# Performance work log

Hardware: AMD Instinct MI355X
Metric: run time of the kernel (lower is better)

## Reference

```python
import jax, jax.numpy as jnp
import numpy as np

B, N, D = 16, 1024, 512
NH = 8
HD = D // NH
K_DEFAULT, K_MAX = 4, 6
PROX_THRESH = 20.0
LN_EPS = 1e-5


def _linear_params(key, din, dout):
    kw, kb = jax.random.split(key)
    lim = 1.0 / np.sqrt(din)
    W = jax.random.uniform(kw, (din, dout), jnp.float32, -lim, lim)
    b = jax.random.uniform(kb, (dout,), jnp.float32, -lim, lim)
    return W, b


def setup_inputs() -> dict:
    key = jax.random.key(0)
    ks = jax.random.split(key, 16)
    agent_repr_1 = jax.random.normal(ks[0], (B, N, D), jnp.float32)
    ego_distance = jax.random.uniform(ks[1], (B, N), jnp.float32) * 100.0  # meters
    ego_mask = jax.random.uniform(ks[2], (B, N), jnp.float32)  # soft ego indicator (torch casts bool->float)
    ego_speed = jax.random.uniform(ks[3], (B,), jnp.float32) * 10.0
    Wq, bq = _linear_params(ks[4], D, D)
    Wk, bk = _linear_params(ks[5], D, D)
    Wv, bv = _linear_params(ks[6], D, D)
    Weq, beq = _linear_params(ks[7], D, D)
    Wek, bek = _linear_params(ks[8], D, D)  # defined in module but unused in forward
    Wev, bev = _linear_params(ks[9], D, D)  # defined in module but unused in forward
    Wd1, bd1 = _linear_params(ks[10], 2, D // 4)
    Wd2, bd2 = _linear_params(ks[11], D // 4, NH)
    ln_g = jnp.ones((D,), jnp.float32)
    ln_b = jnp.zeros((D,), jnp.float32)
    return dict(agent_repr_1=agent_repr_1, ego_distance=ego_distance, ego_mask=ego_mask,
                ego_speed=ego_speed, Wq=Wq, bq=bq, Wk=Wk, bk=bk, Wv=Wv, bv=bv,
                Weq=Weq, beq=beq, Wek=Wek, bek=bek, Wev=Wev, bev=bev,
                Wd1=Wd1, bd1=bd1, Wd2=Wd2, bd2=bd2, ln_g=ln_g, ln_b=ln_b)


def _compute_K(ego_speed, ego_distance):
    # deterministic lookup table; concrete python int (mirrors .item() in torch)
    d = np.asarray(ego_distance)
    s = np.asarray(ego_speed)
    density = (d < PROX_THRESH).astype(np.float32).sum(-1) / max(d.shape[-1], 1)
    K = K_DEFAULT
    if float(s.mean()) > 15.0:
        K = min(K + 1, K_MAX)
    if float(density.mean()) > 0.5:
        K = min(K + 1, K_MAX)
    return K


def _layernorm(x, g, b):
    mu = jnp.mean(x, -1, keepdims=True)
    var = jnp.var(x, -1, keepdims=True)
    return (x - mu) * jax.lax.rsqrt(var + LN_EPS) * g + b


def reference(agent_repr_1, ego_distance, ego_mask, ego_speed,
              Wq, bq, Wk, bk, Wv, bv, Weq, beq, Wek, bek, Wev, bev,
              Wd1, bd1, Wd2, bd2, ln_g, ln_b):
    K = min(_compute_K(ego_speed, ego_distance), N - 1)
    if K <= 0:
        return _layernorm(agent_repr_1, ln_g, ln_b)
    # top-K nearest neighbors by ego distance, excluding self
    dist = jnp.broadcast_to(ego_distance[:, None, :], (B, N, N))  # row i: candidate distances
    dist = jnp.where(jnp.eye(N, dtype=bool)[None], jnp.inf, dist)
    _, topk_idx = jax.lax.top_k(-dist, K)  # [B,N,K] smallest distances
    gathered = jax.vmap(lambda xb, ib: xb[ib])(agent_repr_1, topk_idx)  # [B,N,K,D]
    is_ego = ego_mask[..., None]
    Q = (1.0 - is_ego) * (agent_repr_1 @ Wq + bq) + is_ego * (agent_repr_1 @ Weq + beq)
    Km = gathered @ Wk + bk
    Vm = gathered @ Wv + bv
    Qh = Q.reshape(B, N, NH, HD).transpose(0, 2, 1, 3)          # [B,H,N,hd]
    Kh = Km.reshape(B, N, K, NH, HD).transpose(0, 3, 1, 2, 4)   # [B,H,N,K,hd]
    Vh = Vm.reshape(B, N, K, NH, HD).transpose(0, 3, 1, 2, 4)
    scores = jnp.einsum('bhnd,bhnkd->bhnk', Qh, Kh) / np.sqrt(HD)
    q_dist = jnp.broadcast_to(ego_distance[:, :, None], (B, N, K))
    k_dist = jnp.take_along_axis(jnp.broadcast_to(ego_distance[:, None, :], (B, N, N)), topk_idx, axis=2)
    dist_pair = jnp.stack([q_dist, k_dist], -1)                 # [B,N,K,2]
    bias = jax.nn.relu(dist_pair @ Wd1 + bd1) @ Wd2 + bd2       # [B,N,K,H]
    scores = scores * bias.transpose(0, 3, 1, 2)                # multiplicative distance bias
    attn = jax.nn.softmax(scores, axis=-1)
    attn_out = jnp.einsum('bhnk,bhnkd->bhnd', attn, Vh)
    attn_out = attn_out.transpose(0, 2, 1, 3).reshape(B, N, D)
    return _layernorm(agent_repr_1 + attn_out, ln_g, ln_b)
```

## Files before the change

kernel.cpp:

```cpp
#include <hip/hip_runtime.h>
#include <math.h>

constexpr int CB  = 16;
constexpr int CN  = 1024;
constexpr int CD  = 512;
constexpr int KM1 = 7;
constexpr int RB  = 32;

typedef __attribute__((ext_vector_type(8))) short bf8;
typedef __attribute__((ext_vector_type(4))) float f32x4;
typedef __attribute__((ext_vector_type(4))) unsigned short us4;

__device__ inline float bf2f(unsigned short u) {
    union { unsigned int i; float f; } v; v.i = ((unsigned)u) << 16; return v.f;
}
__device__ inline unsigned short f2bf(float f) {
    union { unsigned int i; float f; } v; v.f = f;
    unsigned r = v.i + 0x7FFFu + ((v.i >> 16) & 1u);
    return (unsigned short)(r >> 16);
}
__device__ inline unsigned int cvtpk(float lo, float hi) {
    unsigned int r;
    asm("v_cvt_pk_bf16_f32 %0, %1, %2" : "=v"(r) : "v"(lo), "v"(hi));
    return r;
}
__device__ inline bf8 pack8(float4 x, float4 y) {
    union { bf8 v; unsigned int u[4]; } r;
    r.u[0] = cvtpk(x.x, x.y); r.u[1] = cvtpk(x.z, x.w);
    r.u[2] = cvtpk(y.x, y.y); r.u[3] = cvtpk(y.z, y.w);
    return r.v;
}
__device__ inline us4 pack4(float4 x) {
    union { us4 v; unsigned int u[2]; } r;
    r.u[0] = cvtpk(x.x, x.y); r.u[1] = cvtpk(x.z, x.w);
    return r.v;
}

__global__ __launch_bounds__(256) void k_pre(
    const float* __restrict__ dist, const float* __restrict__ speed,
    const float* __restrict__ Wk, const float* __restrict__ Wv,
    int* __restrict__ Kout,
    int* __restrict__ candIdx, float* __restrict__ candDist,
    unsigned short* __restrict__ WkT, unsigned short* __restrict__ WvT) {
    int t = threadIdx.x;
    int bid = blockIdx.x;

    if (bid < 16) {
        __shared__ float sdist[CN];
        __shared__ unsigned long long red64[4];
        int b = bid;
        for (int i = t; i < CN; i += 256) sdist[i] = dist[b * CN + i];
        __syncthreads();
        for (int sel = 0; sel < KM1; sel++) {
            unsigned long long best = 0xFFFFFFFFFFFFFFFFull;
            for (int i = t; i < CN; i += 256) {
                unsigned long long key =
                    ((unsigned long long)__float_as_uint(sdist[i]) << 32) | (unsigned)i;
                best = best < key ? best : key;
            }
#pragma unroll
            for (int off = 32; off; off >>= 1) {
                unsigned long long o = __shfl_xor(best, off);
                best = best < o ? best : o;
            }
            if ((t & 63) == 0) red64[t >> 6] = best;
            __syncthreads();
            if (t == 0) {
                unsigned long long m0 = red64[0] < red64[1] ? red64[0] : red64[1];
                unsigned long long m1 = red64[2] < red64[3] ? red64[2] : red64[3];
                unsigned long long m = m0 < m1 ? m0 : m1;
                int idx = (int)(unsigned)(m & 0xFFFFFFFFu);
                candIdx[b * KM1 + sel]  = idx;
                candDist[b * KM1 + sel] = __uint_as_float((unsigned)(m >> 32));
                sdist[idx] = 3.4e38f;
            }
            __syncthreads();
        }
        return;
    }
    if (bid < 144) {
        __shared__ unsigned short tile[64][68];
        int b2 = bid - 16;
        int kt = b2 & 7, ct = (b2 >> 3) & 7, mat = b2 >> 6;
        const float* W = mat ? Wv : Wk;
        unsigned short* WT = mat ? WvT : WkT;
        int k0 = kt * 64, c0 = ct * 64;
#pragma unroll
        for (int p = 0; p < 4; p++) {
            int kr = p * 16 + (t >> 4);
            int cc = (t & 15) * 4;
            float4 v = *(const float4*)(W + (size_t)(k0 + kr) * CD + c0 + cc);
            *(us4*)&tile[kr][cc] = pack4(v);
        }
        __syncthreads();
#pragma unroll
        for (int p = 0; p < 4; p++) {
            int cr = p * 16 + (t >> 4);
            int kk = (t & 15) * 4;
            us4 o;
            o.x = tile[kk + 0][cr];
            o.y = tile[kk + 1][cr];
            o.z = tile[kk + 2][cr];
            o.w = tile[kk + 3][cr];
            *(us4*)(WT + (size_t)(c0 + cr) * CD + k0 + kk) = o;
        }
        return;
    }
    {
        __shared__ int red[256];
        int cnt = 0;
        for (int i = t; i < CB * CN; i += 256) cnt += (dist[i] < 20.0f) ? 1 : 0;
        red[t] = cnt;
        __syncthreads();
        for (int s = 128; s > 0; s >>= 1) {
            if (t < s) red[t] += red[t + s];
            __syncthreads();
        }
        if (t == 0) {
            float ss = 0.f;
            for (int i = 0; i < CB; i++) ss += speed[i];
            int K = 4;
            if (ss / (float)CB > 15.0f) K = (K + 1 > 6) ? 6 : K + 1;
            float density = (float)red[0] / (float)(CB * CN);
            if (density > 0.5f) K = (K + 1 > 6) ? 6 : K + 1;
            if (K > CN - 1) K = CN - 1;
            if (K < 0) K = 0;
            *Kout = K;
        }
    }
}

__global__ __launch_bounds__(256) void k_mid(
    const float* __restrict__ X,
    const unsigned short* __restrict__ WkT, const float* __restrict__ bk,
    const unsigned short* __restrict__ WvT, const float* __restrict__ bv,
    const float* __restrict__ Wq, const float* __restrict__ bq,
    const float* __restrict__ Weq, const float* __restrict__ beq,
    const int* __restrict__ candIdx,
    unsigned short* __restrict__ VcB, float* __restrict__ S0,
    unsigned short* __restrict__ Y,
    unsigned short* __restrict__ X2) {
    int t = threadIdx.x;
    int bid = blockIdx.x;
    __shared__ unsigned short sbuf[RB][520];

    if (bid >= 384) {
        int tileId = bid - 384;
        int b = tileId >> 5, rblk = tileId & 31;
        int row0 = b * CN + rblk * RB;
        for (int idx = t; idx < RB * 128; idx += 256) {
            int r = idx >> 7, c4 = idx & 127;
            float4 xv = *(const float4*)(X + (size_t)(row0 + r) * CD + c4 * 4);
            *(us4*)&sbuf[r][c4 * 4] = pack4(xv);
        }
        __syncthreads();
        unsigned short* dst = X2 + (size_t)tileId * 16384;
#pragma unroll
        for (int it = 0; it < 8; it++) {
            int unit = t + it * 256;
            int r = unit & 31, kg = (unit >> 5) & 3, s = unit >> 7;
            const unsigned short* src = &sbuf[r][s * 32 + kg * 8];
            us4 lo = *(const us4*)src;
            us4 hi = *(const us4*)(src + 4);
            *(us4*)(dst + (size_t)unit * 8)     = lo;
            *(us4*)(dst + (size_t)unit * 8 + 4) = hi;
        }
        return;
    }

    int b = (bid < 128) ? (bid >> 3) : ((bid - 128) >> 4);
    for (int i = t; i < 16 * 128; i += 256) {
        int m = i >> 7, c4 = i & 127;
        float4 xv = {0.f, 0.f, 0.f, 0.f};
        if (m < KM1)
            xv = *(const float4*)(X + (size_t)(b * CN + candIdx[b * KM1 + m]) * CD + c4 * 4);
        *(us4*)&sbuf[m][c4 * 4] = pack4(xv);
    }
    __syncthreads();

    int w = t >> 6, lane = t & 63, lr = lane & 15, kg = lane >> 4;

    if (bid < 128) {
        int ny = bid & 7;
        int c = ny * 64 + w * 16 + lr;
        const unsigned short* wtp = WvT + (size_t)c * CD + kg * 8;
        f32x4 acc = {0.f, 0.f, 0.f, 0.f};
#pragma unroll
        for (int s = 0; s < 16; s++) {
            bf8 bfr = *(const bf8*)(wtp + s * 32);
            bf8 a   = *(const bf8*)&sbuf[lr][s * 32 + kg * 8];
            acc = __builtin_amdgcn_mfma_f32_16x16x32_bf16(a, bfr, acc, 0, 0, 0);
        }
        float bv_ = bv[c];
#pragma unroll
        for (int q = 0; q < 4; q++) {
            int m = kg * 4 + q;
            if (m < KM1)
                VcB[(size_t)(b * KM1 + m) * CD + c] = f2bf(acc[q] + bv_);
        }
        return;
    }

    int rem = (bid - 128) & 15;
    int h = rem >> 1, half = rem & 1;
    __shared__ unsigned short sKc16[16][68];
    __shared__ float sKcf[KM1][64];

    {
        int c = h * 64 + w * 16 + lr;
        const unsigned short* wtp = WkT + (size_t)c * CD + kg * 8;
        f32x4 acc = {0.f, 0.f, 0.f, 0.f};
#pragma unroll
        for (int s = 0; s < 16; s++) {
            bf8 bfr = *(const bf8*)(wtp + s * 32);
            bf8 a   = *(const bf8*)&sbuf[lr][s * 32 + kg * 8];
            acc = __builtin_amdgcn_mfma_f32_16x16x32_bf16(a, bfr, acc, 0, 0, 0);
        }
        float bk_ = bk[c];
        int cl = w * 16 + lr;
#pragma unroll
        for (int q = 0; q < 4; q++) {
            int m = kg * 4 + q;
            float val = (m < KM1) ? (acc[q] + bk_) : 0.f;
            sKc16[m][cl] = f2bf(val);
            if (m < KM1) sKcf[m][cl] = val;
        }
    }
    __syncthreads();

    if (half == 0 && t < 14) {
        int mat = t / 7, m = t % 7;
        const float* bias = mat ? beq : bq;
        float s = 0.f;
        for (int c = 0; c < 64; c++) s = fmaf(bias[h * 64 + c], sKcf[m][c], s);
        S0[((b * 2 + mat) * KM1 + m) * 8 + h] = s;
    }

    bf8 a0 = *(const bf8*)&sKc16[lr][kg * 8];
    bf8 a1 = *(const bf8*)&sKc16[lr][32 + kg * 8];
    unsigned short* Y2b = Y + (size_t)b * 64 * 112 * 8;
#pragma unroll
    for (int mat = 0; mat < 2; mat++) {
        const float* W = mat ? Weq : Wq;
#pragma unroll
        for (int nt = 0; nt < 4; nt++) {
            int n0 = (half * 16 + w * 4 + nt) * 16;
            const float* wp = W + (size_t)(n0 + lr) * CD + h * 64 + kg * 8;
            float4 f0 = *(const float4*)(wp);
            float4 f1 = *(const float4*)(wp + 4);
            float4 f2 = *(const float4*)(wp + 32);
            float4 f3 = *(const float4*)(wp + 36);
            f32x4 acc = {0.f, 0.f, 0.f, 0.f};
            acc = __builtin_amdgcn_mfma_f32_16x16x32_bf16(a0, pack8(f0, f1), acc, 0, 0, 0);
            acc = __builtin_amdgcn_mfma_f32_16x16x32_bf16(a1, pack8(f2, f3), acc, 0, 0, 0);
            int k_out = n0 + lr;
            int k8 = k_out >> 3, krem = k_out & 7;
#pragma unroll
            for (int q = 0; q < 4; q++) {
                int m = kg * 4 + q;
                if (m < KM1) {
                    int n = mat * 56 + m * 8 + h;
                    Y2b[((size_t)k8 * 112 + n) * 8 + krem] = f2bf(acc[q]);
                }
            }
        }
    }
}

__global__ __launch_bounds__(512) void k_attn(
    const float* __restrict__ X, const float* __restrict__ dist,
    const float* __restrict__ mask,
    const float* __restrict__ Wd1, const float* __restrict__ bd1,
    const float* __restrict__ Wd2, const float* __restrict__ bd2,
    const float* __restrict__ lng, const float* __restrict__ lnb,
    const int* __restrict__ Kp, const int* __restrict__ candIdx,
    const float* __restrict__ candDist,
    const unsigned short* __restrict__ VcB, const float* __restrict__ S0,
    const unsigned short* __restrict__ Y,
    const unsigned short* __restrict__ X2, int useX2,
    float* __restrict__ out) {

    __shared__ float sS[RB][116];
    __shared__ unsigned short sVc[KM1][520];
    __shared__ float sW7[RB][8][8];
    __shared__ float sBias[RB][6][2][8];
    __shared__ int   snbr[RB][6];
    __shared__ float skd[RB][6];
    __shared__ float srd[RB];
    __shared__ float sE[RB];
    __shared__ float sS0[112];

    int t = threadIdx.x;
    int hw = blockIdx.x;
    int bid = (hw & 7) * 64 + (hw >> 3);
    int b = bid >> 5, rblk = bid & 31;
    int row0 = b * CN + rblk * RB;
    int K = *Kp;

    for (int idx = t; idx < KM1 * 128; idx += 512) {
        int m = idx >> 7, c4 = idx & 127;
        *(us4*)&sVc[m][c4 * 4] =
            *(const us4*)(VcB + (size_t)(b * KM1 + m) * CD + c4 * 4);
    }
    if (t < 112) sS0[t] = S0[b * 112 + t];
    if (t < RB) {
        int i = rblk * RB + t;
        sE[t]  = mask[b * CN + i];
        srd[t] = dist[b * CN + i];
        int cnt = 0;
        for (int m = 0; m <= K && cnt < K; m++) {
            int c = candIdx[b * KM1 + m];
            if (c != i) { snbr[t][cnt] = m; skd[t][cnt] = candDist[b * KM1 + m]; cnt++; }
        }
    }
    __syncthreads();

    int w = t >> 6;
    if (w < 4) {
        int lane = t & 63, lr = lane & 15, kg = lane >> 4;
        f32x4 acc00 = {0.f, 0.f, 0.f, 0.f}, acc10 = acc00, acc01 = acc00, acc11 = acc00;
        bool has2 = (w < 3);
        const unsigned short* ypk = Y + ((size_t)b * 64 * 112 + (size_t)kg * 112 + (w * 16 + lr)) * 8;
        __builtin_amdgcn_s_setprio(1);
        if (useX2) {
            const unsigned short* x2s = X2 + (size_t)bid * 16384 + kg * 256 + lr * 8;
#pragma unroll
            for (int s = 0; s < 16; s++) {
                const unsigned short* xp = x2s + s * 1024;
                bf8 a0 = *(const bf8*)xp;
                bf8 a1 = *(const bf8*)(xp + 128);
                const unsigned short* ys = ypk + (size_t)s * 4 * 112 * 8;
                bf8 b0 = *(const bf8*)ys;
                acc00 = __builtin_amdgcn_mfma_f32_16x16x32_bf16(a0, b0, acc00, 0, 0, 0);
                acc10 = __builtin_amdgcn_mfma_f32_16x16x32_bf16(a1, b0, acc10, 0, 0, 0);
                if (has2) {
                    bf8 b1 = *(const bf8*)(ys + 512);
                    acc01 = __builtin_amdgcn_mfma_f32_16x16x32_bf16(a0, b1, acc01, 0, 0, 0);
                    acc11 = __builtin_amdgcn_mfma_f32_16x16x32_bf16(a1, b1, acc11, 0, 0, 0);
                }
            }
        } else {
            const float* x0 = X + (size_t)(row0 + lr) * CD + kg * 8;
            const float* x1 = X + (size_t)(row0 + 16 + lr) * CD + kg * 8;
#pragma unroll
            for (int s = 0; s < 16; s++) {
                int k0 = s * 32;
                float4 xa0 = *(const float4*)(x0 + k0);
                float4 xb0 = *(const float4*)(x0 + k0 + 4);
                float4 xa1 = *(const float4*)(x1 + k0);
                float4 xb1 = *(const float4*)(x1 + k0 + 4);
                bf8 a0 = pack8(xa0, xb0);
                bf8 a1 = pack8(xa1, xb1);
                const unsigned short* ys = ypk + (size_t)s * 4 * 112 * 8;
                bf8 b0 = *(const bf8*)ys;
                acc00 = __builtin_amdgcn_mfma_f32_16x16x32_bf16(a0, b0, acc00, 0, 0, 0);
                acc10 = __builtin_amdgcn_mfma_f32_16x16x32_bf16(a1, b0, acc10, 0, 0, 0);
                if (has2) {
                    bf8 b1 = *(const bf8*)(ys + 512);
                    acc01 = __builtin_amdgcn_mfma_f32_16x16x32_bf16(a0, b1, acc01, 0, 0, 0);
                    acc11 = __builtin_amdgcn_mfma_f32_16x16x32_bf16(a1, b1, acc11, 0, 0, 0);
                }
            }
        }
        __builtin_amdgcn_s_setprio(0);
        int n0 = w * 16 + lr;
#pragma unroll
        for (int q = 0; q < 4; q++) {
            sS[kg * 4 + q][n0]      = acc00[q];
            sS[16 + kg * 4 + q][n0] = acc10[q];
        }
        if (has2) {
            int n1 = (w + 4) * 16 + lr;
#pragma unroll
            for (int q = 0; q < 4; q++) {
                sS[kg * 4 + q][n1]      = acc01[q];
                sS[16 + kg * 4 + q][n1] = acc11[q];
            }
        }
    } else {
        int tot2 = RB * K * 2;
        for (int task = t - 256; task < tot2; task += 256) {
            int half = task & 1;
            int pid = task >> 1;
            int r = pid / K, k = pid - r * K;
            int j0 = half * 64;
            float qd = srd[r], kd = skd[r][k];
            float bacc[8];
#pragma unroll
            for (int h = 0; h < 8; h++) bacc[h] = 0.f;
            for (int j = j0; j < j0 + 64; j++) {
                float hid = fmaf(qd, Wd1[j], fmaf(kd, Wd1[128 + j], bd1[j]));
                hid = fmaxf(hid, 0.f);
                float4 wa = *(const float4*)(Wd2 + j * 8);
                float4 wb = *(const float4*)(Wd2 + j * 8 + 4);
                bacc[0] = fmaf(hid, wa.x, bacc[0]);
                bacc[1] = fmaf(hid, wa.y, bacc[1]);
                bacc[2] = fmaf(hid, wa.z, bacc[2]);
                bacc[3] = fmaf(hid, wa.w, bacc[3]);
                bacc[4] = fmaf(hid, wb.x, bacc[4]);
                bacc[5] = fmaf(hid, wb.y, bacc[5]);
                bacc[6] = fmaf(hid, wb.z, bacc[6]);
                bacc[7] = fmaf(hid, wb.w, bacc[7]);
            }
#pragma unroll
            for (int h = 0; h < 8; h++) sBias[r][k][half][h] = bacc[h];
        }
    }
    __syncthreads();

    if (t < RB * 8) {
        int r = t >> 3, h = t & 7;
        float e = sE[r];
        float wv[6];
#pragma unroll
        for (int k = 0; k < 6; k++) {
            if (k < K) {
                int m = snbr[r][k];
                float scq = sS[r][m * 8 + h]      + sS0[m * 8 + h];
                float sce = sS[r][56 + m * 8 + h] + sS0[56 + m * 8 + h];
                float sc = (1.f - e) * scq + e * sce;
                float bias = sBias[r][k][0][h] + sBias[r][k][1][h] + bd2[h];
                wv[k] = sc * 0.125f * bias;
            } else {
                wv[k] = -3.4e38f;
            }
        }
        float mx = -3.4e38f;
#pragma unroll
        for (int k = 0; k < 6; k++) mx = fmaxf(mx, wv[k]);
        float sum = 0.f;
#pragma unroll
        for (int k = 0; k < 6; k++) {
            wv[k] = __expf(wv[k] - mx);
            sum += wv[k];
        }
        float inv = 1.f / sum;
#pragma unroll
        for (int m = 0; m < KM1; m++) {
            float acc = 0.f;
#pragma unroll
            for (int k = 0; k < 6; k++) {
                bool use = (k < K) && (snbr[r][k] == m);
                acc += use ? wv[k] * inv : 0.f;
            }
            sW7[r][h][m] = acc;
        }
    }
    __syncthreads();

    {
        int r = t >> 4, tr = t & 15;
        const float* xrow = X + (size_t)(row0 + r) * CD;
        float4 vals[8];
        float sum = 0.f, sq = 0.f;
#pragma unroll
        for (int j = 0; j < 8; j++) {
            int d = tr * 4 + j * 64;
            float ax = 0.f, ay = 0.f, az = 0.f, aw = 0.f;
#pragma unroll
            for (int m = 0; m < KM1; m++) {
                float wgt = sW7[r][j][m];
                us4 vv = *(const us4*)&sVc[m][d];
                ax = fmaf(wgt, bf2f(vv.x), ax);
                ay = fmaf(wgt, bf2f(vv.y), ay);
                az = fmaf(wgt, bf2f(vv.z), az);
                aw = fmaf(wgt, bf2f(vv.w), aw);
            }
            float4 xv = *(const float4*)(xrow + d);
            float4 v;
            v.x = xv.x + ax; v.y = xv.y + ay; v.z = xv.z + az; v.w = xv.w + aw;
            vals[j] = v;
            sum += v.x + v.y + v.z + v.w;
            sq = fmaf(v.x, v.x, sq); sq = fmaf(v.y, v.y, sq);
            sq = fmaf(v.z, v.z, sq); sq = fmaf(v.w, v.w, sq);
        }
        sum += __shfl_xor(sum, 1, 16); sq += __shfl_xor(sq, 1, 16);
        sum += __shfl_xor(sum, 2, 16); sq += __shfl_xor(sq, 2, 16);
        sum += __shfl_xor(sum, 4, 16); sq += __shfl_xor(sq, 4, 16);
        sum += __shfl_xor(sum, 8, 16); sq += __shfl_xor(sq, 8, 16);
        float mu  = sum * (1.f / 512.f);
        float var = sq * (1.f / 512.f) - mu * mu;
        float inv = rsqrtf(var + 1e-5f);
        float* orow = out + (size_t)(row0 + r) * CD;
#pragma unroll
        for (int j = 0; j < 8; j++) {
            int d = tr * 4 + j * 64;
            float4 g  = *(const float4*)(lng + d);
            float4 bb = *(const float4*)(lnb + d);
            float4 v = vals[j];
            float4 o;
            o.x = (v.x - mu) * inv * g.x + bb.x;
            o.y = (v.y - mu) * inv * g.y + bb.y;
            o.z = (v.z - mu) * inv * g.z + bb.z;
            o.w = (v.w - mu) * inv * g.w + bb.w;
            *(float4*)(orow + d) = o;
        }
    }
}

extern "C" void kernel_launch(void* const* d_in, const int* in_sizes, int n_in,
                              void* d_out, int out_size, void* d_ws, size_t ws_size,
                              hipStream_t stream) {
    (void)in_sizes; (void)n_in; (void)out_size;
    const float* X     = (const float*)d_in[0];
    const float* dist  = (const float*)d_in[1];
    const float* mask  = (const float*)d_in[2];
    const float* speed = (const float*)d_in[3];
    const float* Wq    = (const float*)d_in[4];
    const float* bq    = (const float*)d_in[5];
    const float* Wk    = (const float*)d_in[6];
    const float* bk    = (const float*)d_in[7];
    const float* Wv    = (const float*)d_in[8];
    const float* bv    = (const float*)d_in[9];
    const float* Weq   = (const float*)d_in[10];
    const float* beq   = (const float*)d_in[11];
    const float* Wd1   = (const float*)d_in[16];
    const float* bd1   = (const float*)d_in[17];
    const float* Wd2   = (const float*)d_in[18];
    const float* bd2   = (const float*)d_in[19];
    const float* lng   = (const float*)d_in[20];
    const float* lnb   = (const float*)d_in[21];
    float* out = (float*)d_out;

    char* ws = (char*)d_ws;
    int*   Kp       = (int*)(ws);
    int*   candIdx  = (int*)(ws + 256);
    float* candDist = (float*)(ws + 1024);
    float* S0       = (float*)(ws + 2048);
    unsigned short* VcB = (unsigned short*)(ws + 245760);
    unsigned short* Y   = (unsigned short*)(ws + 475136);
    unsigned short* WkT = (unsigned short*)(ws + 2310144);
    unsigned short* WvT = (unsigned short*)(ws + 2834432);
    unsigned short* X2  = (unsigned short*)(ws + 3358720);
    int useX2 = (ws_size >= (size_t)3358720 + 16777216) ? 1 : 0;

    k_pre<<<145, 256, 0, stream>>>(dist, speed, Wk, Wv, Kp, candIdx, candDist, WkT, WvT);
    int midBlocks = 384 + (useX2 ? 512 : 0);
    k_mid<<<midBlocks, 256, 0, stream>>>(X, WkT, bk, WvT, bv, Wq, bq, Weq, beq,
                                         candIdx, VcB, S0, Y, X2);
    k_attn<<<CB * (CN / RB), 512, 0, stream>>>(X, dist, mask, Wd1, bd1, Wd2, bd2, lng, lnb,
                                               Kp, candIdx, candDist, VcB, S0, Y,
                                               X2, useX2, out);
}
```

Measured before the change: 70.85 us.

## Precompute distance-bias MLP in mid kernel and spread score MFMAs across seven waves

Moves the per-pair distance-bias MLP out of the attention kernel into 64 extra blocks of the middle kernel, which write a global bias buffer in workspace. This frees waves 4-6 of the attention kernel, so the score GEMM is now spread over seven waves with one N-tile each instead of four waves with two. The goal is to shorten the attention kernel's critical path by overlapping the bias work with the mid-kernel GEMMs. The cost is an extra 3 MB global buffer write and read. The new path is only taken when the workspace is large enough, otherwise the old path runs.

```diff
diff --git a/kernel.cpp b/kernel.cpp
--- a/kernel.cpp
+++ b/kernel.cpp
@@ -131,18 +131,61 @@
 }
 
 __global__ __launch_bounds__(256) void k_mid(
-    const float* __restrict__ X,
+    const float* __restrict__ X, const float* __restrict__ dist,
     const unsigned short* __restrict__ WkT, const float* __restrict__ bk,
     const unsigned short* __restrict__ WvT, const float* __restrict__ bv,
     const float* __restrict__ Wq, const float* __restrict__ bq,
     const float* __restrict__ Weq, const float* __restrict__ beq,
-    const int* __restrict__ candIdx,
+    const float* __restrict__ Wd1, const float* __restrict__ bd1,
+    const float* __restrict__ Wd2, const float* __restrict__ bd2,
+    const int* __restrict__ Kp, const int* __restrict__ candIdx,
+    const float* __restrict__ candDist,
     unsigned short* __restrict__ VcB, float* __restrict__ S0,
     unsigned short* __restrict__ Y,
-    unsigned short* __restrict__ X2) {
+    unsigned short* __restrict__ X2, float* __restrict__ gBias,
+    int biasBase) {
     int t = threadIdx.x;
     int bid = blockIdx.x;
     __shared__ unsigned short sbuf[RB][520];
+
+    if (bid >= biasBase) {
+        int g = (bid - biasBase) * 256 + t;
+        int b = g >> 10, i = g & 1023;
+        int K = *Kp;
+        float qd = dist[g];
+        int   nb[6]; float kd6[6];
+#pragma unroll
+        for (int j = 0; j < 6; j++) { nb[j] = 0; kd6[j] = 0.f; }
+        int cnt = 0;
+        for (int m = 0; m <= K && cnt < K; m++) {
+            int c = candIdx[b * KM1 + m];
+            if (c != i) { nb[cnt] = m; kd6[cnt] = candDist[b * KM1 + m]; cnt++; }
+        }
+        for (int k = 0; k < K; k++) {
+            float kd = kd6[k];
+            float bacc[8];
+#pragma unroll
+            for (int h = 0; h < 8; h++) bacc[h] = bd2[h];
+            for (int j = 0; j < 128; j++) {
+                float hid = fmaf(qd, Wd1[j], fmaf(kd, Wd1[128 + j], bd1[j]));
+                hid = fmaxf(hid, 0.f);
+                float4 wa = *(const float4*)(Wd2 + j * 8);
+                float4 wb = *(const float4*)(Wd2 + j * 8 + 4);
+                bacc[0] = fmaf(hid, wa.x, bacc[0]);
+                bacc[1] = fmaf(hid, wa.y, bacc[1]);
+                bacc[2] = fmaf(hid, wa.z, bacc[2]);
+                bacc[3] = fmaf(hid, wa.w, bacc[3]);
+                bacc[4] = fmaf(hid, wb.x, bacc[4]);
+                bacc[5] = fmaf(hid, wb.y, bacc[5]);
+                bacc[6] = fmaf(hid, wb.z, bacc[6]);
+                bacc[7] = fmaf(hid, wb.w, bacc[7]);
+            }
+            float* dst = gBias + ((size_t)g * 6 + k) * 8;
+#pragma unroll
+            for (int h = 0; h < 8; h++) dst[h] = bacc[h];
+        }
+        return;
+    }
 
     if (bid >= 384) {
         int tileId = bid - 384;
@@ -278,6 +321,7 @@
     const unsigned short* __restrict__ VcB, const float* __restrict__ S0,
     const unsigned short* __restrict__ Y,
     const unsigned short* __restrict__ X2, int useX2,
+    const float* __restrict__ gBias, int useBias,
     float* __restrict__ out) {
 
     __shared__ float sS[RB][116];
@@ -316,94 +360,133 @@
     __syncthreads();
 
     int w = t >> 6;
-    if (w < 4) {
-        int lane = t & 63, lr = lane & 15, kg = lane >> 4;
-        f32x4 acc00 = {0.f, 0.f, 0.f, 0.f}, acc10 = acc00, acc01 = acc00, acc11 = acc00;
-        bool has2 = (w < 3);
-        const unsigned short* ypk = Y + ((size_t)b * 64 * 112 + (size_t)kg * 112 + (w * 16 + lr)) * 8;
-        __builtin_amdgcn_s_setprio(1);
-        if (useX2) {
-            const unsigned short* x2s = X2 + (size_t)bid * 16384 + kg * 256 + lr * 8;
-#pragma unroll
-            for (int s = 0; s < 16; s++) {
-                const unsigned short* xp = x2s + s * 1024;
-                bf8 a0 = *(const bf8*)xp;
-                bf8 a1 = *(const bf8*)(xp + 128);
-                const unsigned short* ys = ypk + (size_t)s * 4 * 112 * 8;
-                bf8 b0 = *(const bf8*)ys;
-                acc00 = __builtin_amdgcn_mfma_f32_16x16x32_bf16(a0, b0, acc00, 0, 0, 0);
-                acc10 = __builtin_amdgcn_mfma_f32_16x16x32_bf16(a1, b0, acc10, 0, 0, 0);
-                if (has2) {
-                    bf8 b1 = *(const bf8*)(ys + 512);
-                    acc01 = __builtin_amdgcn_mfma_f32_16x16x32_bf16(a0, b1, acc01, 0, 0, 0);
-                    acc11 = __builtin_amdgcn_mfma_f32_16x16x32_bf16(a1, b1, acc11, 0, 0, 0);
+    if (useBias) {
+        if (w < 7) {
+            int lane = t & 63, lr = lane & 15, kg = lane >> 4;
+            f32x4 acc00 = {0.f, 0.f, 0.f, 0.f}, acc10 = acc00;
+            const unsigned short* ypk =
+                Y + ((size_t)b * 64 * 112 + (size_t)kg * 112 + (w * 16 + lr)) * 8;
+            __builtin_amdgcn_s_setprio(1);
+            if (useX2) {
+                const unsigned short* x2s =
+                    X2 + (size_t)bid * 16384 + kg * 256 + lr * 8;
+#pragma unroll
+                for (int s = 0; s < 16; s++) {
+                    const unsigned short* xp = x2s + s * 1024;
+                    bf8 a0 = *(const bf8*)xp;
+                    bf8 a1 = *(const bf8*)(xp + 128);
+                    bf8 b0 = *(const bf8*)(ypk + (size_t)s * 4 * 112 * 8);
+                    acc00 = __builtin_amdgcn_mfma_f32_16x16x32_bf16(a0, b0, acc00, 0, 0, 0);
+                    acc10 = __builtin_amdgcn_mfma_f32_16x16x32_bf16(a1, b0, acc10, 0, 0, 0);
                 }
+            } else {
+                const float* x0 = X + (size_t)(row0 + lr) * CD + kg * 8;
+                const float* x1 = X + (size_t)(row0 + 16 + lr) * CD + kg * 8;
+#pragma unroll
+                for (int s = 0; s < 16; s++) {
+                    int k0 = s * 32;
+                    bf8 a0 = pack8(*(const float4*)(x0 + k0), *(const float4*)(x0 + k0 + 4));
+                    bf8 a1 = pack8(*(const float4*)(x1 + k0), *(const float4*)(x1 + k0 + 4));
+                    bf8 b0 = *(const bf8*)(ypk + (size_t)s * 4 * 112 * 8);
+                    acc00 = __builtin_amdgcn_mfma_f32_16x16x32_bf16(a0, b0, acc00, 0, 0, 0);
+                    acc10 = __builtin_amdgcn_mfma_f32_16x16x32_bf16(a1, b0, acc10, 0, 0, 0);
+                }
+            }
+            __builtin_amdgcn_s_setprio(0);
+            int n0 = w * 16 + lr;
+#pragma unroll
+            for (int q = 0; q < 4; q++) {
+                sS[kg * 4 + q][n0]      = acc00[q];
+                sS[16 + kg * 4 + q][n0] = acc10[q];
+            }
+        }
+    } else {
+        if (w < 4) {
+            int lane = t & 63, lr = lane & 15, kg = lane >> 4;
+            f32x4 acc00 = {0.f, 0.f, 0.f, 0.f}, acc10 = acc00, acc01 = acc00, acc11 = acc00;
+            bool has2 = (w < 3);
+            const unsigned short* ypk =
+                Y + ((size_t)b * 64 * 112 + (size_t)kg * 112 + (w * 16 + lr)) * 8;
+            __builtin_amdgcn_s_setprio(1);
+            if (useX2) {
+                const unsigned short* x2s = X2 + (size_t)bid * 16384 + kg * 256 + lr * 8;
+#pragma unroll
+                for (int s = 0; s < 16; s++) {
+                    const unsigned short* xp = x2s + s * 1024;
+                    bf8 a0 = *(const bf8*)xp;
+                    bf8 a1 = *(const bf8*)(xp + 128);
+                    const unsigned short* ys = ypk + (size_t)s * 4 * 112 * 8;
+                    bf8 b0 = *(const bf8*)ys;
+                    acc00 = __builtin_amdgcn_mfma_f32_16x16x32_bf16(a0, b0, acc00, 0, 0, 0);
+                    acc10 = __builtin_amdgcn_mfma_f32_16x16x32_bf16(a1, b0, acc10, 0, 0, 0);
+                    if (has2) {
+                        bf8 b1 = *(const bf8*)(ys + 512);
+                        acc01 = __builtin_amdgcn_mfma_f32_16x16x32_bf16(a0, b1, acc01, 0, 0, 0);
+                        acc11 = __builtin_amdgcn_mfma_f32_16x16x32_bf16(a1, b1, acc11, 0, 0, 0);
+                    }
+                }
+            } else {
+                const float* x0 = X + (size_t)(row0 + lr) * CD + kg * 8;
+                const float* x1 = X + (size_t)(row0 + 16 + lr) * CD + kg * 8;
+#pragma unroll
+                for (int s = 0; s < 16; s++) {
+                    int k0 = s * 32;
+                    bf8 a0 = pack8(*(const float4*)(x0 + k0), *(const float4*)(x0 + k0 + 4));
+                    bf8 a1 = pack8(*(const float4*)(x1 + k0), *(const float4*)(x1 + k0 + 4));
+                    const unsigned short* ys = ypk + (size_t)s * 4 * 112 * 8;
+                    bf8 b0 = *(const bf8*)ys;
+                    acc00 = __builtin_amdgcn_mfma_f32_16x16x32_bf16(a0, b0, acc00, 0, 0, 0);
+                    acc10 = __builtin_amdgcn_mfma_f32_16x16x32_bf16(a1, b0, acc10, 0, 0, 0);
+                    if (has2) {
+                        bf8 b1 = *(const bf8*)(ys + 512);
+                        acc01 = __builtin_amdgcn_mfma_f32_16x16x32_bf16(a0, b1, acc01, 0, 0, 0);
+                        acc11 = __builtin_amdgcn_mfma_f32_16x16x32_bf16(a1, b1, acc11, 0, 0, 0);
+                    }
+                }
+            }
+            __builtin_amdgcn_s_setprio(0);
+            int n0 = w * 16 + lr;
+#pragma unroll
+            for (int q = 0; q < 4; q++) {
+                sS[kg * 4 + q][n0]      = acc00[q];
+                sS[16 + kg * 4 + q][n0] = acc10[q];
+            }
+            if (has2) {
+                int n1 = (w + 4) * 16 + lr;
+#pragma unroll
+                for (int q = 0; q < 4; q++) {
+                    sS[kg * 4 + q][n1]      = acc01[q];
+                    sS[16 + kg * 4 + q][n1] = acc11[q];
+                }
             }
         } else {
-            const float* x0 = X + (size_t)(row0 + lr) * CD + kg * 8;
-            const float* x1 = X + (size_t)(row0 + 16 + lr) * CD + kg * 8;
-#pragma unroll
-            for (int s = 0; s < 16; s++) {
-                int k0 = s * 32;
-                float4 xa0 = *(const float4*)(x0 + k0);
-                float4 xb0 = *(const float4*)(x0 + k0 + 4);
-                float4 xa1 = *(const float4*)(x1 + k0);
-                float4 xb1 = *(const float4*)(x1 + k0 + 4);
-                bf8 a0 = pack8(xa0, xb0);
-                bf8 a1 = pack8(xa1, xb1);
-                const unsigned short* ys = ypk + (size_t)s * 4 * 112 * 8;
-                bf8 b0 = *(const bf8*)ys;
-                acc00 = __builtin_amdgcn_mfma_f32_16x16x32_bf16(a0, b0, acc00, 0, 0, 0);
-                acc10 = __builtin_amdgcn_mfma_f32_16x16x32_bf16(a1, b0, acc10, 0, 0, 0);
-                if (has2) {
-                    bf8 b1 = *(const bf8*)(ys + 512);
-                    acc01 = __builtin_amdgcn_mfma_f32_16x16x32_bf16(a0, b1, acc01, 0, 0, 0);
-                    acc11 = __builtin_amdgcn_mfma_f32_16x16x32_bf16(a1, b1, acc11, 0, 0, 0);
+            int tot2 = RB * K * 2;
+            for (int task = t - 256; task < tot2; task += 256) {
+                int half = task & 1;
+                int pid = task >> 1;
+                int r = pid / K, k = pid - r * K;
+                int j0 = half * 64;
+                float qd = srd[r], kd = skd[r][k];
+                float bacc[8];
+#pragma unroll
+                for (int h = 0; h < 8; h++) bacc[h] = 0.f;
+                for (int j = j0; j < j0 + 64; j++) {
+                    float hid = fmaf(qd, Wd1[j], fmaf(kd, Wd1[128 + j], bd1[j]));
+                    hid = fmaxf(hid, 0.f);
+                    float4 wa = *(const float4*)(Wd2 + j * 8);
+                    float4 wb = *(const float4*)(Wd2 + j * 8 + 4);
+                    bacc[0] = fmaf(hid, wa.x, bacc[0]);
+                    bacc[1] = fmaf(hid, wa.y, bacc[1]);
+                    bacc[2] = fmaf(hid, wa.z, bacc[2]);
+                    bacc[3] = fmaf(hid, wa.w, bacc[3]);
+                    bacc[4] = fmaf(hid, wb.x, bacc[4]);
+                    bacc[5] = fmaf(hid, wb.y, bacc[5]);
+                    bacc[6] = fmaf(hid, wb.z, bacc[6]);
+                    bacc[7] = fmaf(hid, wb.w, bacc[7]);
                 }
-            }
-        }
-        __builtin_amdgcn_s_setprio(0);
-        int n0 = w * 16 + lr;
-#pragma unroll
-        for (int q = 0; q < 4; q++) {
-            sS[kg * 4 + q][n0]      = acc00[q];
-            sS[16 + kg * 4 + q][n0] = acc10[q];
-        }
-        if (has2) {
-            int n1 = (w + 4) * 16 + lr;
-#pragma unroll
-            for (int q = 0; q < 4; q++) {
-                sS[kg * 4 + q][n1]      = acc01[q];
-                sS[16 + kg * 4 + q][n1] = acc11[q];
-            }
-        }
-    } else {
-        int tot2 = RB * K * 2;
-        for (int task = t - 256; task < tot2; task += 256) {
-            int half = task & 1;
-            int pid = task >> 1;
-            int r = pid / K, k = pid - r * K;
-            int j0 = half * 64;
-            float qd = srd[r], kd = skd[r][k];
-            float bacc[8];
-#pragma unroll
-            for (int h = 0; h < 8; h++) bacc[h] = 0.f;
-            for (int j = j0; j < j0 + 64; j++) {
-                float hid = fmaf(qd, Wd1[j], fmaf(kd, Wd1[128 + j], bd1[j]));
-                hid = fmaxf(hid, 0.f);
-                float4 wa = *(const float4*)(Wd2 + j * 8);
-                float4 wb = *(const float4*)(Wd2 + j * 8 + 4);
-                bacc[0] = fmaf(hid, wa.x, bacc[0]);
-                bacc[1] = fmaf(hid, wa.y, bacc[1]);
-                bacc[2] = fmaf(hid, wa.z, bacc[2]);
-                bacc[3] = fmaf(hid, wa.w, bacc[3]);
-                bacc[4] = fmaf(hid, wb.x, bacc[4]);
-                bacc[5] = fmaf(hid, wb.y, bacc[5]);
-                bacc[6] = fmaf(hid, wb.z, bacc[6]);
-                bacc[7] = fmaf(hid, wb.w, bacc[7]);
-            }
-#pragma unroll
-            for (int h = 0; h < 8; h++) sBias[r][k][half][h] = bacc[h];
+#pragma unroll
+                for (int h = 0; h < 8; h++) sBias[r][k][half][h] = bacc[h];
+            }
         }
     }
     __syncthreads();
@@ -411,6 +494,7 @@
     if (t < RB * 8) {
         int r = t >> 3, h = t & 7;
         float e = sE[r];
+        const float* gb = gBias + ((size_t)(row0 + r) * 6) * 8 + h;
         float wv[6];
 #pragma unroll
         for (int k = 0; k < 6; k++) {
@@ -419,7 +503,8 @@
                 float scq = sS[r][m * 8 + h]      + sS0[m * 8 + h];
                 float sce = sS[r][56 + m * 8 + h] + sS0[56 + m * 8 + h];
                 float sc = (1.f - e) * scq + e * sce;
-                float bias = sBias[r][k][0][h] + sBias[r][k][1][h] + bd2[h];
+                float bias = useBias ? gb[k * 8]
+                                     : (sBias[r][k][0][h] + sBias[r][k][1][h] + bd2[h]);
                 wv[k] = sc * 0.125f * bias;
             } else {
                 wv[k] = -3.4e38f;
@@ -532,13 +617,17 @@
     unsigned short* WkT = (unsigned short*)(ws + 2310144);
     unsigned short* WvT = (unsigned short*)(ws + 2834432);
     unsigned short* X2  = (unsigned short*)(ws + 3358720);
-    int useX2 = (ws_size >= (size_t)3358720 + 16777216) ? 1 : 0;
+    float* gBias        = (float*)(ws + 20135936);
+    int useX2   = (ws_size >= (size_t)3358720 + 16777216) ? 1 : 0;
+    int useBias = (ws_size >= (size_t)20135936 + 3145728) ? 1 : 0;
 
     k_pre<<<145, 256, 0, stream>>>(dist, speed, Wk, Wv, Kp, candIdx, candDist, WkT, WvT);
-    int midBlocks = 384 + (useX2 ? 512 : 0);
-    k_mid<<<midBlocks, 256, 0, stream>>>(X, WkT, bk, WvT, bv, Wq, bq, Weq, beq,
-                                         candIdx, VcB, S0, Y, X2);
+    int biasBase = 384 + (useX2 ? 512 : 0);
+    int midBlocks = biasBase + (useBias ? 64 : 0);
+    k_mid<<<midBlocks, 256, 0, stream>>>(X, dist, WkT, bk, WvT, bv, Wq, bq, Weq, beq,
+                                         Wd1, bd1, Wd2, bd2, Kp, candIdx, candDist,
+                                         VcB, S0, Y, X2, gBias, biasBase);
     k_attn<<<CB * (CN / RB), 512, 0, stream>>>(X, dist, mask, Wd1, bd1, Wd2, bd2, lng, lnb,
                                                Kp, candIdx, candDist, VcB, S0, Y,
-                                               X2, useX2, out);
-}
+                                               X2, useX2, gBias, useBias, out);
+}
```

Result: faster. 67.91 us (-4.2%).
